# Kernel tuning notes

Hardware: AMD Instinct MI355X
Metric: run time of the kernel (lower is better)

Reference implementation:

```python
import jax, jax.numpy as jnp
import numpy as np

B, S, D = 2, 2048, 2048
RANK = 512
N_HEADS = 16
DROPOUT_RATE = 0.1
KEEP = 1.0 - DROPOUT_RATE  # original safe_dropout scales by 1/keep even when deterministic


def setup_inputs() -> dict:
    key = jax.random.key(0)
    ks = jax.random.split(key, 9)
    return {
        "x": jax.random.normal(ks[0], (B, S, D), jnp.float32),
        "g_Q": jax.random.uniform(ks[1], (B, S, RANK), jnp.float32),
        "g_K": jax.random.uniform(ks[2], (B, S, RANK), jnp.float32),
        "g_V": jax.random.uniform(ks[3], (B, S, RANK), jnp.float32),
        "qk_read": jax.random.normal(ks[4], (RANK, D), jnp.float32) * 0.02,
        "qk_write": jax.random.normal(ks[5], (RANK, D), jnp.float32) * 0.02,
        "v_read": jax.random.normal(ks[6], (RANK, D), jnp.float32) * 0.02,
        "v_write": jax.random.normal(ks[7], (RANK, D), jnp.float32) * 0.02,
        "W_O": jax.random.normal(ks[8], (D, D), jnp.float32) * 0.02,
    }


def _gated_lowrank(x, g, rd, wr):
    # g * (x @ rd.T) @ wr : [B,S,D] -> [B,S,rank] -> [B,S,D]
    return (g * jnp.einsum('bsd,rd->bsr', x, rd)) @ wr


def reference(x, g_Q, g_K, g_V, qk_read, qk_write, v_read, v_write, W_O):
    Bx, Sx, Dx = x.shape
    d_head = Dx // N_HEADS

    Q = _gated_lowrank(x, g_Q, qk_read, qk_write)
    K = _gated_lowrank(x, g_K, qk_read, qk_write)
    V = _gated_lowrank(x, g_V, v_read, v_write)

    Q = Q.reshape(Bx, Sx, N_HEADS, d_head).transpose(0, 2, 1, 3)
    K = K.reshape(Bx, Sx, N_HEADS, d_head).transpose(0, 2, 1, 3)
    V = V.reshape(Bx, Sx, N_HEADS, d_head).transpose(0, 2, 1, 3)

    scale = jnp.sqrt(jnp.float32(d_head))
    scores = jnp.einsum('bhsd,bhtd->bhst', Q, K) / scale  # [B,H,S,S]
    causal = jnp.tril(jnp.ones((Sx, Sx), dtype=jnp.bool_))
    scores = jnp.where(causal, scores, jnp.finfo(scores.dtype).min)
    attn_w = jax.nn.softmax(scores, axis=-1)
    attn_w = attn_w / KEEP  # deterministic branch of original safe_dropout

    out = jnp.einsum('bhst,bhtd->bhsd', attn_w, V)
    out = out.transpose(0, 2, 1, 3).reshape(Bx, Sx, Dx)
    out = out @ W_O
    out = out / KEEP  # deterministic dropout scaling
    return out
```

## Files before the change

kernel.cpp:

```cpp
#include <hip/hip_runtime.h>
#include <cstdint>
#include <cstddef>

typedef unsigned short u16;
typedef unsigned int u32;
typedef __attribute__((ext_vector_type(4))) float f32x4;
typedef __attribute__((ext_vector_type(8))) __bf16 bf16x8;
typedef __attribute__((ext_vector_type(8))) u16 u16x8;
typedef __attribute__((ext_vector_type(4))) u16 u16x4;

__device__ __forceinline__ u16 f2bf(float x) {
  u32 u = __builtin_bit_cast(u32, x);
  u += 0x7fffu + ((u >> 16) & 1u);
  return (u16)(u >> 16);
}
__device__ __forceinline__ u16 f2bf_trunc(float x) {
  return (u16)(__builtin_bit_cast(u32, x) >> 16);
}
__device__ __forceinline__ float bf2f(u16 b) {
  return __builtin_bit_cast(float, (u32)b << 16);
}
__device__ __forceinline__ bf16x8 ldfrag(const u16* p) {
  return __builtin_bit_cast(bf16x8, *(const u16x8*)p);
}
__device__ __forceinline__ void gload_lds16(const void* g, void* l) {
  auto gp = (const __attribute__((address_space(1))) u32*)g;
  auto lp = (__attribute__((address_space(3))) u32*)l;
  __builtin_amdgcn_global_load_lds(gp, lp, 16, 0, 0);
}
#define MFMA16(a, b, c) __builtin_amdgcn_mfma_f32_16x16x32_bf16(a, b, c, 0, 0, 0)


__global__ void cvt_kernel(const float* __restrict__ in, u16* __restrict__ out, int n) {
  int i = (blockIdx.x * blockDim.x + threadIdx.x) * 4;
  if (i >= n) return;
  f32x4 v = *(const f32x4*)(in + i);
  u16x4 r = { f2bf(v[0]), f2bf(v[1]), f2bf(v[2]), f2bf(v[3]) };
  *(u16x4*)(out + i) = r;
}

__global__ void tcvt_kernel(const float* __restrict__ in, u16* __restrict__ out, int R, int C) {
  __shared__ float tile[32][33];
  int bx = blockIdx.x * 32, by = blockIdx.y * 32;
  int tx = threadIdx.x, ty = threadIdx.y;
#pragma unroll
  for (int i = 0; i < 32; i += 8)
    tile[ty + i][tx] = in[(size_t)(by + ty + i) * C + bx + tx];
  __syncthreads();
#pragma unroll
  for (int i = 0; i < 32; i += 8)
    out[(size_t)(bx + ty + i) * R + by + tx] = f2bf(tile[tx][ty + i]);
}

__global__ void gate_kernel(const float* __restrict__ gq, const float* __restrict__ gk,
                            const float* __restrict__ gv, const u16* __restrict__ Pcat,
                            u16* __restrict__ Aq, u16* __restrict__ Ak, u16* __restrict__ Av,
                            int n) {
  int i = (blockIdx.x * blockDim.x + threadIdx.x) * 4;
  if (i >= n) return;
  int s = i >> 9;
  int r = i & 511;
  u16x4 pq = *(const u16x4*)(Pcat + (size_t)s * 1024 + r);
  u16x4 pv = *(const u16x4*)(Pcat + (size_t)s * 1024 + 512 + r);
  f32x4 q = *(const f32x4*)(gq + i);
  f32x4 k = *(const f32x4*)(gk + i);
  f32x4 v = *(const f32x4*)(gv + i);
  u16x4 aq, ak, av;
#pragma unroll
  for (int j = 0; j < 4; ++j) {
    float pf = bf2f(pq[j]);
    float vf = bf2f(pv[j]);
    aq[j] = f2bf(q[j] * pf);
    ak[j] = f2bf(k[j] * pf);
    av[j] = f2bf(v[j] * vf);
  }
  *(u16x4*)(Aq + i) = aq;
  *(u16x4*)(Ak + i) = ak;
  *(u16x4*)(Av + i) = av;
}

template <bool F32OUT>
__global__ void gemm_bt(const u16* __restrict__ A, const u16* __restrict__ Bt,
                        void* __restrict__ Cp, int M, int N, int K, float scale) {
  __shared__ u16 Al[128 * 32];
  __shared__ u16 Bl[128 * 32];
  const int tid = threadIdx.x;
  const int lane = tid & 63;
  const int w = tid >> 6;
  const int wr = (w >> 1) * 64;
  const int wc = (w & 1) * 64;
  const size_t bm = (size_t)blockIdx.y * 128;
  const size_t bn = (size_t)blockIdx.x * 128;

  f32x4 acc[4][4] = {};

  const int srow = lane >> 2;
  const int sch = lane & 3;
  const int kc = lane >> 4;
  const int rl = lane & 15;

  for (int kt = 0; kt < K; kt += 32) {
#pragma unroll
    for (int half = 0; half < 2; ++half) {
      int rb = half * 64 + w * 16;
      int row = rb + srow;
      int ch = sch ^ ((row >> 1) & 3);
      gload_lds16(A + (bm + row) * (size_t)K + kt + ch * 8, &Al[rb * 32]);
    }
#pragma unroll
    for (int half = 0; half < 2; ++half) {
      int rb = half * 64 + w * 16;
      int row = rb + srow;
      int ch = sch ^ ((row >> 1) & 3);
      gload_lds16(Bt + (bn + row) * (size_t)K + kt + ch * 8, &Bl[rb * 32]);
    }
    asm volatile("s_waitcnt vmcnt(0)" ::: "memory");
    __syncthreads();

    bf16x8 af[4], bfr[4];
#pragma unroll
    for (int m = 0; m < 4; ++m) {
      int row = wr + m * 16 + rl;
      af[m] = ldfrag(&Al[row * 32 + (kc ^ ((row >> 1) & 3)) * 8]);
    }
#pragma unroll
    for (int n = 0; n < 4; ++n) {
      int row = wc + n * 16 + rl;
      bfr[n] = ldfrag(&Bl[row * 32 + (kc ^ ((row >> 1) & 3)) * 8]);
    }
#pragma unroll
    for (int m = 0; m < 4; ++m)
#pragma unroll
      for (int n = 0; n < 4; ++n)
        acc[m][n] = MFMA16(af[m], bfr[n], acc[m][n]);
    __syncthreads();
  }

  const int r0 = (lane >> 4) * 4;
#pragma unroll
  for (int m = 0; m < 4; ++m) {
    size_t grow = bm + wr + m * 16 + r0;
#pragma unroll
    for (int n = 0; n < 4; ++n) {
      size_t gcol = bn + wc + n * 16 + rl;
#pragma unroll
      for (int r = 0; r < 4; ++r) {
        float v = acc[m][n][r] * scale;
        if constexpr (F32OUT)
          ((float*)Cp)[(grow + r) * (size_t)N + gcol] = v;
        else
          ((u16*)Cp)[(grow + r) * (size_t)N + gcol] = f2bf(v);
      }
    }
  }
}

__global__ __launch_bounds__(256, 3) void attn_kernel(const u16* __restrict__ Q,
                                                      const u16* __restrict__ Kg,
                                                      const u16* __restrict__ Vt,
                                                      u16* __restrict__ AO) {
  __shared__ u16 Kl[2][64 * 128];
  __shared__ u16 Vl[128 * 64];

  const int tid = threadIdx.x;
  const int lane = tid & 63;
  const int w = tid >> 6;
  const int bh = blockIdx.x;
  const int qb = 31 - blockIdx.y;
  const int b = bh >> 4;
  const int h = bh & 15;

  const int rl = lane & 15;
  const int g4 = lane >> 4;

  const float SC = 0.1275255128608411f;
  const float THR = 10.0f;

  bf16x8 ones;
  {
    u16x8 ou;
#pragma unroll
    for (int j = 0; j < 8; ++j) ou[j] = 0x3F80;
    ones = __builtin_bit_cast(bf16x8, ou);
  }

  auto stageK = [&](int buf, int t0) {
    int roff = lane >> 4;
    int cch = lane & 15;
#pragma unroll
    for (int i = 0; i < 4; ++i) {
      int rb = w * 16 + i * 4;
      int row = rb + roff;
      int ch = cch ^ (row & 7);
      gload_lds16(Kg + ((size_t)b * 2048 + t0 + row) * 2048 + h * 128 + ch * 8,
                  &Kl[buf][rb * 128]);
    }
  };
  auto stageV = [&](int t0) {
    int roff = lane >> 3;
    int cch = lane & 7;
#pragma unroll
    for (int i = 0; i < 4; ++i) {
      int rb = w * 32 + i * 8;
      int row = rb + roff;
      int ch = cch ^ (row & 7);
      gload_lds16(Vt + (size_t)(h * 128 + row) * 4096 + (size_t)b * 2048 + t0 + ch * 8,
                  &Vl[rb * 64]);
    }
  };

  const int ntiles = qb + 1;
  const int qbase = qb * 64 + w * 16;
  const size_t qrow0 = (size_t)b * 2048 + (size_t)qb * 64;

  bf16x8 qf[4];
  {
    const u16* qp = Q + (qrow0 + w * 16 + rl) * 2048 + h * 128 + g4 * 8;
#pragma unroll
    for (int ks = 0; ks < 4; ++ks) qf[ks] = ldfrag(qp + ks * 32);
  }

  float m_r[4], l_r[4];
#pragma unroll
  for (int r = 0; r < 4; ++r) { m_r[r] = -3.0e38f; l_r[r] = 0.f; }
  f32x4 oacc[8] = {};

  stageK(0, 0);
  __syncthreads();
  int cur = 0;

#pragma unroll 1
  for (int t = 0; t < ntiles; ++t) {
    const int t0 = t * 64;
    stageV(t0);
    const bool pref = (t + 1 < ntiles);
    if (pref) stageK(cur ^ 1, (t + 1) * 64);

    float p[4][4];
    float pmax[4] = {-3.0e38f, -3.0e38f, -3.0e38f, -3.0e38f};
    __builtin_amdgcn_s_setprio(1);
#pragma unroll
    for (int nf = 0; nf < 4; ++nf) {
      f32x4 c = {};
      int trow = nf * 16 + rl;
#pragma unroll
      for (int ks = 0; ks < 4; ++ks) {
        bf16x8 kf = ldfrag(&Kl[cur][trow * 128 + ((ks * 4 + g4) ^ (trow & 7)) * 8]);
        c = MFMA16(qf[ks], kf, c);
      }
      if (t == qb) {
        int tc = t0 + nf * 16 + rl;
        int fragq = qbase + g4 * 4;
#pragma unroll
        for (int r = 0; r < 4; ++r)
          p[nf][r] = (tc <= fragq + r) ? c[r] * SC : -3.0e38f;
      } else {
#pragma unroll
        for (int r = 0; r < 4; ++r) p[nf][r] = c[r] * SC;
      }
#pragma unroll
      for (int r = 0; r < 4; ++r) pmax[r] = fmaxf(pmax[r], p[nf][r]);
    }
    __builtin_amdgcn_s_setprio(0);

#pragma unroll
    for (int off = 1; off < 16; off <<= 1)
#pragma unroll
      for (int r = 0; r < 4; ++r)
        pmax[r] = fmaxf(pmax[r], __shfl_xor(pmax[r], off, 16));

    float mg = -3.0e38f;
#pragma unroll
    for (int r = 0; r < 4; ++r) mg = fmaxf(mg, pmax[r] - m_r[r]);
    if (__any(mg > THR)) {
#pragma unroll
      for (int r = 0; r < 4; ++r) {
        float mn = fmaxf(m_r[r], pmax[r]);
        float alpha = exp2f(m_r[r] - mn);
        m_r[r] = mn;
        l_r[r] *= alpha;
#pragma unroll
        for (int nf = 0; nf < 8; ++nf) oacc[nf][r] *= alpha;
      }
    }

    u16 ebf[4][4];
#pragma unroll
    for (int nf = 0; nf < 4; ++nf)
#pragma unroll
      for (int r = 0; r < 4; ++r)
        ebf[nf][r] = f2bf_trunc(exp2f(p[nf][r] - m_r[r]));

    if (pref) asm volatile("s_waitcnt vmcnt(4)\n\ts_barrier" ::: "memory");
    else      asm volatile("s_waitcnt vmcnt(0)\n\ts_barrier" ::: "memory");

    u16* pl = &Kl[cur][w * 1024];
#pragma unroll
    for (int nf = 0; nf < 4; ++nf) {
      int tt = nf * 16 + rl;
#pragma unroll
      for (int r = 0; r < 4; ++r) {
        int q = g4 * 4 + r;
        pl[q * 64 + ((tt >> 3) ^ (q & 7)) * 8 + (tt & 7)] = ebf[nf][r];
      }
    }

    __builtin_amdgcn_s_setprio(1);
    f32x4 rs = {};
#pragma unroll
    for (int ks = 0; ks < 2; ++ks) {
      bf16x8 pa = ldfrag(&pl[rl * 64 + ((ks * 4 + g4) ^ (rl & 7)) * 8]);
#pragma unroll
      for (int nf = 0; nf < 8; ++nf) {
        int drow = nf * 16 + rl;
        bf16x8 vf = ldfrag(&Vl[drow * 64 + ((ks * 4 + g4) ^ (drow & 7)) * 8]);
        oacc[nf] = MFMA16(pa, vf, oacc[nf]);
      }
      rs = MFMA16(pa, ones, rs);
    }
    __builtin_amdgcn_s_setprio(0);
#pragma unroll
    for (int r = 0; r < 4; ++r) l_r[r] += rs[r];

    __syncthreads();
    cur ^= 1;
  }

#pragma unroll
  for (int nf = 0; nf < 8; ++nf) {
    size_t dc = (size_t)h * 128 + nf * 16 + rl;
#pragma unroll
    for (int r = 0; r < 4; ++r) {
      float v = oacc[nf][r] / l_r[r];
      AO[(qrow0 + w * 16 + g4 * 4 + r) * 2048 + dc] = f2bf(v);
    }
  }
}


extern "C" void kernel_launch(void* const* d_in, const int* in_sizes, int n_in,
                              void* d_out, int out_size, void* d_ws, size_t ws_size,
                              hipStream_t stream) {
  const float* x = (const float*)d_in[0];
  const float* gQ = (const float*)d_in[1];
  const float* gK = (const float*)d_in[2];
  const float* gV = (const float*)d_in[3];
  const float* qkr = (const float*)d_in[4];
  const float* qkw = (const float*)d_in[5];
  const float* vr = (const float*)d_in[6];
  const float* vw = (const float*)d_in[7];
  const float* wo = (const float*)d_in[8];
  float* out = (float*)d_out;

  u16* p = (u16*)d_ws;
  u16* x_bf = p;   p += 8388608;
  u16* qkr_b = p;  p += 1048576;
  u16* vr_b = p;   p += 1048576;
  u16* qkwT = p;   p += 1048576;
  u16* vwT = p;    p += 1048576;
  u16* woT = p;    p += 4194304;
  u16* Pcat = p;   p += 4194304;
  u16* Aq = p;     p += 2097152;
  u16* Ak = p;     p += 2097152;
  u16* Av = p;     p += 2097152;
  u16* Qb = p;     p += 8388608;
  u16* Kb = p;     p += 8388608;
  u16* Vt = x_bf;
  u16* AO = Qb;

  cvt_kernel<<<8192, 256, 0, stream>>>(x, x_bf, 8388608);
  cvt_kernel<<<1024, 256, 0, stream>>>(qkr, qkr_b, 1048576);
  cvt_kernel<<<1024, 256, 0, stream>>>(vr, vr_b, 1048576);
  tcvt_kernel<<<dim3(64, 16), dim3(32, 8), 0, stream>>>(qkw, qkwT, 512, 2048);
  tcvt_kernel<<<dim3(64, 16), dim3(32, 8), 0, stream>>>(vw, vwT, 512, 2048);
  tcvt_kernel<<<dim3(64, 64), dim3(32, 8), 0, stream>>>(wo, woT, 2048, 2048);

  gemm_bt<false><<<dim3(8, 32), 256, 0, stream>>>(x_bf, qkr_b, Pcat, 4096, 1024, 2048, 1.f);

  gate_kernel<<<2048, 256, 0, stream>>>(gQ, gK, gV, Pcat, Aq, Ak, Av, 2097152);

  gemm_bt<false><<<dim3(16, 64), 256, 0, stream>>>(Aq, qkwT, Qb, 8192, 2048, 512, 1.f);

  gemm_bt<false><<<dim3(32, 16), 256, 0, stream>>>(vwT, Av, Vt, 2048, 4096, 512, 1.f);

  attn_kernel<<<dim3(32, 32), 256, 0, stream>>>(Qb, Kb, Vt, AO);

  gemm_bt<true><<<dim3(16, 32), 256, 0, stream>>>(AO, woT, out, 4096, 2048, 2048,
                                                  1.2345679012345678f);
}
```

Before: 247.6 us.

## Transpose QK^T MFMA output so P writes to LDS are vectorized per query row

Swaps the MFMA operand order so each lane holds four consecutive key scores for a single query row. The row max then needs only two cross-lane shuffles instead of per-register 16-lane reductions, the running max becomes one scalar per lane, and P is packed into 64-bit LDS stores instead of scattered 16-bit writes. The softmax scale is folded into the Q gating kernel so the per-score multiply disappears. The rescale path now needs shuffles to hand alpha back to the output layout, and the rounding of Q changes slightly.

```diff
diff --git a/kernel.cpp b/kernel.cpp
--- a/kernel.cpp
+++ b/kernel.cpp
@@ -8,14 +8,12 @@
 typedef __attribute__((ext_vector_type(8))) __bf16 bf16x8;
 typedef __attribute__((ext_vector_type(8))) u16 u16x8;
 typedef __attribute__((ext_vector_type(4))) u16 u16x4;
+typedef __attribute__((ext_vector_type(2))) u32 u32x2;
 
 __device__ __forceinline__ u16 f2bf(float x) {
   u32 u = __builtin_bit_cast(u32, x);
   u += 0x7fffu + ((u >> 16) & 1u);
   return (u16)(u >> 16);
-}
-__device__ __forceinline__ u16 f2bf_trunc(float x) {
-  return (u16)(__builtin_bit_cast(u32, x) >> 16);
 }
 __device__ __forceinline__ float bf2f(u16 b) {
   return __builtin_bit_cast(float, (u32)b << 16);
@@ -56,6 +54,7 @@
                             const float* __restrict__ gv, const u16* __restrict__ Pcat,
                             u16* __restrict__ Aq, u16* __restrict__ Ak, u16* __restrict__ Av,
                             int n) {
+  const float SC = 0.1275255128608411f;
   int i = (blockIdx.x * blockDim.x + threadIdx.x) * 4;
   if (i >= n) return;
   int s = i >> 9;
@@ -70,7 +69,7 @@
   for (int j = 0; j < 4; ++j) {
     float pf = bf2f(pq[j]);
     float vf = bf2f(pv[j]);
-    aq[j] = f2bf(q[j] * pf);
+    aq[j] = f2bf(q[j] * SC * pf);
     ak[j] = f2bf(k[j] * pf);
     av[j] = f2bf(v[j] * vf);
   }
@@ -173,7 +172,6 @@
   const int rl = lane & 15;
   const int g4 = lane >> 4;
 
-  const float SC = 0.1275255128608411f;
   const float THR = 10.0f;
 
   bf16x8 ones;
@@ -210,7 +208,7 @@
   };
 
   const int ntiles = qb + 1;
-  const int qbase = qb * 64 + w * 16;
+  const int qq = qb * 64 + w * 16 + rl;
   const size_t qrow0 = (size_t)b * 2048 + (size_t)qb * 64;
 
   bf16x8 qf[4];
@@ -220,9 +218,10 @@
     for (int ks = 0; ks < 4; ++ks) qf[ks] = ldfrag(qp + ks * 32);
   }
 
-  float m_r[4], l_r[4];
-#pragma unroll
-  for (int r = 0; r < 4; ++r) { m_r[r] = -3.0e38f; l_r[r] = 0.f; }
+  float m_r = -3.0e38f;
+  float l_r[4];
+#pragma unroll
+  for (int r = 0; r < 4; ++r) l_r[r] = 0.f;
   f32x4 oacc[8] = {};
 
   stageK(0, 0);
@@ -237,7 +236,6 @@
     if (pref) stageK(cur ^ 1, (t + 1) * 64);
 
     float p[4][4];
-    float pmax[4] = {-3.0e38f, -3.0e38f, -3.0e38f, -3.0e38f};
     __builtin_amdgcn_s_setprio(1);
 #pragma unroll
     for (int nf = 0; nf < 4; ++nf) {
@@ -246,50 +244,51 @@
 #pragma unroll
       for (int ks = 0; ks < 4; ++ks) {
         bf16x8 kf = ldfrag(&Kl[cur][trow * 128 + ((ks * 4 + g4) ^ (trow & 7)) * 8]);
-        c = MFMA16(qf[ks], kf, c);
+        c = MFMA16(kf, qf[ks], c);
       }
       if (t == qb) {
-        int tc = t0 + nf * 16 + rl;
-        int fragq = qbase + g4 * 4;
+        int tb = t0 + nf * 16 + g4 * 4;
 #pragma unroll
         for (int r = 0; r < 4; ++r)
-          p[nf][r] = (tc <= fragq + r) ? c[r] * SC : -3.0e38f;
+          p[nf][r] = (tb + r <= qq) ? c[r] : -3.0e38f;
       } else {
 #pragma unroll
-        for (int r = 0; r < 4; ++r) p[nf][r] = c[r] * SC;
-      }
-#pragma unroll
-      for (int r = 0; r < 4; ++r) pmax[r] = fmaxf(pmax[r], p[nf][r]);
+        for (int r = 0; r < 4; ++r) p[nf][r] = c[r];
+      }
     }
     __builtin_amdgcn_s_setprio(0);
 
-#pragma unroll
-    for (int off = 1; off < 16; off <<= 1)
-#pragma unroll
-      for (int r = 0; r < 4; ++r)
-        pmax[r] = fmaxf(pmax[r], __shfl_xor(pmax[r], off, 16));
-
-    float mg = -3.0e38f;
-#pragma unroll
-    for (int r = 0; r < 4; ++r) mg = fmaxf(mg, pmax[r] - m_r[r]);
-    if (__any(mg > THR)) {
+    float mx = p[0][0];
+#pragma unroll
+    for (int nf = 0; nf < 4; ++nf)
+#pragma unroll
+      for (int r = 0; r < 4; ++r) mx = fmaxf(mx, p[nf][r]);
+    mx = fmaxf(mx, __shfl_xor(mx, 16));
+    mx = fmaxf(mx, __shfl_xor(mx, 32));
+
+    if (__any(mx - m_r > THR)) {
+      float mn = fmaxf(m_r, mx);
+      float alpha = exp2f(m_r - mn);
+      m_r = mn;
 #pragma unroll
       for (int r = 0; r < 4; ++r) {
-        float mn = fmaxf(m_r[r], pmax[r]);
-        float alpha = exp2f(m_r[r] - mn);
-        m_r[r] = mn;
-        l_r[r] *= alpha;
-#pragma unroll
-        for (int nf = 0; nf < 8; ++nf) oacc[nf][r] *= alpha;
-      }
-    }
-
-    u16 ebf[4][4];
-#pragma unroll
-    for (int nf = 0; nf < 4; ++nf)
-#pragma unroll
-      for (int r = 0; r < 4; ++r)
-        ebf[nf][r] = f2bf_trunc(exp2f(p[nf][r] - m_r[r]));
+        float av = __shfl(alpha, g4 * 4 + r, 16);
+        l_r[r] *= av;
+#pragma unroll
+        for (int nf = 0; nf < 8; ++nf) oacc[nf][r] *= av;
+      }
+    }
+
+    u32x2 pk[4];
+#pragma unroll
+    for (int nf = 0; nf < 4; ++nf) {
+      u32 e0 = __builtin_bit_cast(u32, exp2f(p[nf][0] - m_r));
+      u32 e1 = __builtin_bit_cast(u32, exp2f(p[nf][1] - m_r));
+      u32 e2 = __builtin_bit_cast(u32, exp2f(p[nf][2] - m_r));
+      u32 e3 = __builtin_bit_cast(u32, exp2f(p[nf][3] - m_r));
+      pk[nf][0] = (e1 & 0xffff0000u) | (e0 >> 16);
+      pk[nf][1] = (e3 & 0xffff0000u) | (e2 >> 16);
+    }
 
     if (pref) asm volatile("s_waitcnt vmcnt(4)\n\ts_barrier" ::: "memory");
     else      asm volatile("s_waitcnt vmcnt(0)\n\ts_barrier" ::: "memory");
@@ -297,12 +296,8 @@
     u16* pl = &Kl[cur][w * 1024];
 #pragma unroll
     for (int nf = 0; nf < 4; ++nf) {
-      int tt = nf * 16 + rl;
-#pragma unroll
-      for (int r = 0; r < 4; ++r) {
-        int q = g4 * 4 + r;
-        pl[q * 64 + ((tt >> 3) ^ (q & 7)) * 8 + (tt & 7)] = ebf[nf][r];
-      }
+      int c8 = ((nf * 2 + (g4 >> 1)) ^ (rl & 7)) * 8 + (g4 & 1) * 4;
+      *(u32x2*)(&pl[rl * 64 + c8]) = pk[nf];
     }
 
     __builtin_amdgcn_s_setprio(1);
```

Measured after the change: 227.2 us. 8.2% less time.
